# Optimization experiments

Measured on AMD Instinct MI355X. Metric: run time of the kernel, lower is better.

## Reference

```python
import jax, jax.numpy as jnp
import numpy as np

N = 100000          # nodes
E = 1600000         # edges
IN_FEATS = 128
OUT_FEATS = 32      # per head
NUM_HEADS = 8
NEG_SLOPE = 0.2     # DGL GATConv default leaky_relu slope


def setup_inputs() -> dict:
    key = jax.random.key(0)
    k_feat, k_src, k_dst, k_w, k_al, k_ar = jax.random.split(key, 6)
    feat = jax.random.normal(k_feat, (N, IN_FEATS), dtype=jnp.float32)
    src = jax.random.randint(k_src, (E,), 0, N, dtype=jnp.int32)
    dst = jax.random.randint(k_dst, (E,), 0, N, dtype=jnp.int32)
    # learned params of GATConv (fc weight, attn vectors, output bias)
    W = jax.random.normal(k_w, (IN_FEATS, NUM_HEADS * OUT_FEATS), dtype=jnp.float32) * 0.05
    attn_l = jax.random.normal(k_al, (NUM_HEADS, OUT_FEATS), dtype=jnp.float32) * 0.05
    attn_r = jax.random.normal(k_ar, (NUM_HEADS, OUT_FEATS), dtype=jnp.float32) * 0.05
    bias = jnp.zeros((NUM_HEADS * OUT_FEATS,), dtype=jnp.float32)
    return {"feat": feat, "src": src, "dst": dst, "W": W,
            "attn_l": attn_l, "attn_r": attn_r, "bias": bias}


def reference(feat, src, dst, W, attn_l, attn_r, bias):
    # Linear projection: [N, H, D]
    ft = (feat @ W).reshape(N, NUM_HEADS, OUT_FEATS)
    # Per-node attention logit halves: [N, H]
    el = jnp.einsum('nhd,hd->nh', ft, attn_l)
    er = jnp.einsum('nhd,hd->nh', ft, attn_r)
    # Per-edge raw score: [E, H]
    e = jax.nn.leaky_relu(el[src] + er[dst], NEG_SLOPE)
    # Edge softmax over incoming edges of each dst node (segment softmax)
    e_max = jax.ops.segment_max(e, dst, num_segments=N)          # [N, H]
    e_exp = jnp.exp(e - e_max[dst])                              # [E, H]
    e_sum = jax.ops.segment_sum(e_exp, dst, num_segments=N)     # [N, H]
    a = e_exp / e_sum[dst]                                       # [E, H]
    # Weighted message aggregation: [N, H, D]
    msg = ft[src] * a[:, :, None]                                # [E, H, D]
    rst = jax.ops.segment_sum(msg, dst, num_segments=N)
    rst = rst + bias.reshape(NUM_HEADS, OUT_FEATS)
    # Head mean (wrapper): [N, D]
    h = rst.mean(axis=1)
    attn = a[:, :, None]                                         # [E, H, 1] as in DGL
    return (h, attn)
```

## Files before the change

### kernel.cpp

```cpp
#include <hip/hip_runtime.h>
#include <hip/hip_bf16.h>

#define NN 100000
#define NE 1600000
#define KF 128
#define CT 256
#define NH 8
#define SL 56
#define GB 1563

typedef __attribute__((ext_vector_type(8))) short short8;
typedef __attribute__((ext_vector_type(4))) float f32x4;

__device__ __forceinline__ float bf2f(unsigned short u) {
  union { unsigned int i; float f; } x; x.i = ((unsigned int)u) << 16; return x.f;
}
__device__ __forceinline__ unsigned short f2bf(float f) {
  unsigned int b = __float_as_uint(f);
  b += 0x7fffu + ((b >> 16) & 1u);
  return (unsigned short)(b >> 16);
}
__device__ __forceinline__ float lrelu(float e) { return (e > 0.f) ? e : 0.2f * e; }

__global__ void k_wconv(const float* __restrict__ W, unsigned short* __restrict__ Wt) {
  int i = blockIdx.x * 256 + threadIdx.x;
  if (i < KF * CT) {
    int k = i >> 8, c = i & 255;
    Wt[c * KF + k] = f2bf(W[i]);
  }
}

__global__ __launch_bounds__(256) void k_uber(
    const float* __restrict__ feat, const unsigned short* __restrict__ Wt,
    const float* __restrict__ attn_l, const float* __restrict__ attn_r,
    unsigned short* __restrict__ ftb, float* __restrict__ el, float* __restrict__ ei,
    const int* __restrict__ src, const int* __restrict__ dst,
    int* __restrict__ cnt, int* __restrict__ csr)
{
  __shared__ unsigned short fs[64][136];
  const int bid = blockIdx.x;
  const int tid = threadIdx.x;

  if (bid & 1) {
    const int stride = GB * 256;
    for (int e = (bid >> 1) * 256 + tid; e < NE; e += stride) {
      int d = dst[e];
      int sv = src[e];
      int p = atomicAdd(&cnt[d << 4], 1);
      if (p < SL) csr[d * SL + p] = sv;
    }
    return;
  }

  const int lane = tid & 63, w = tid >> 6;
  const int row0 = (bid >> 1) * 64;

  for (int i = tid; i < 64 * 32; i += 256) {
    int r = i >> 5, c4 = (i & 31) * 4;
    int gr = row0 + r;
    float4 v = make_float4(0.f, 0.f, 0.f, 0.f);
    if (gr < NN) v = *(const float4*)(feat + (size_t)gr * KF + c4);
    *(ushort4*)(&fs[r][c4]) = make_ushort4(f2bf(v.x), f2bf(v.y), f2bf(v.z), f2bf(v.w));
  }

  const int bc = lane & 15;
  const int bk = (lane >> 4) * 8;
  short8 bfrag[4][4];
#pragma unroll
  for (int ks = 0; ks < 4; ks++)
#pragma unroll
    for (int n = 0; n < 4; n++)
      bfrag[ks][n] = *(const short8*)(Wt + (size_t)(w * 64 + n * 16 + bc) * KF + ks * 32 + bk);

  __syncthreads();

  f32x4 acc[4][4];
#pragma unroll
  for (int m = 0; m < 4; m++)
#pragma unroll
    for (int n = 0; n < 4; n++) acc[m][n] = (f32x4){0.f, 0.f, 0.f, 0.f};

#pragma unroll
  for (int ks = 0; ks < 4; ks++) {
    short8 af[4];
#pragma unroll
    for (int m = 0; m < 4; m++)
      af[m] = *(const short8*)(&fs[m * 16 + bc][ks * 32 + bk]);
#pragma unroll
    for (int m = 0; m < 4; m++)
#pragma unroll
      for (int n = 0; n < 4; n++)
        acc[m][n] = __builtin_amdgcn_mfma_f32_16x16x32_bf16(af[m], bfrag[ks][n], acc[m][n], 0, 0, 0);
  }

  const int rbase = (lane >> 4) * 4;

#pragma unroll
  for (int m = 0; m < 4; m++) {
#pragma unroll
    for (int r = 0; r < 4; r++) {
      int gr = row0 + m * 16 + rbase + r;
      if (gr < NN) {
        unsigned short* op = ftb + (size_t)gr * CT + w * 64 + bc;
#pragma unroll
        for (int n = 0; n < 4; n++) op[n * 16] = f2bf(acc[m][n][r]);
      }
    }
  }

  float al[4], ar[4];
#pragma unroll
  for (int n = 0; n < 4; n++) {
    al[n] = attn_l[w * 64 + n * 16 + bc];
    ar[n] = attn_r[w * 64 + n * 16 + bc];
  }
#pragma unroll
  for (int m = 0; m < 4; m++) {
#pragma unroll
    for (int r = 0; r < 4; r++) {
      float pl0 = acc[m][0][r] * al[0] + acc[m][1][r] * al[1];
      float pl1 = acc[m][2][r] * al[2] + acc[m][3][r] * al[3];
      float pr0 = acc[m][0][r] * ar[0] + acc[m][1][r] * ar[1];
      float pr1 = acc[m][2][r] * ar[2] + acc[m][3][r] * ar[3];
#pragma unroll
      for (int d = 1; d < 16; d <<= 1) {
        pl0 += __shfl_xor(pl0, d);
        pl1 += __shfl_xor(pl1, d);
        pr0 += __shfl_xor(pr0, d);
        pr1 += __shfl_xor(pr1, d);
      }
      if (bc == 0) {
        int gr = row0 + m * 16 + rbase + r;
        if (gr < NN) {
          *(float2*)(el + (size_t)gr * NH + 2 * w) = make_float2(pl0, pl1);
          *(float2*)(ei + (size_t)gr * 16 + 2 * w) = make_float2(pr0, pr1);
        }
      }
    }
  }
}

__global__ __launch_bounds__(256) void k_edge(
    const int* __restrict__ cnt, const int* __restrict__ csr,
    const float* __restrict__ el, float* __restrict__ ei,
    const unsigned short* __restrict__ ftb, const float* __restrict__ bias,
    float* __restrict__ hout)
{
  const int wid = threadIdx.x >> 6;
  const int lane = threadIdx.x & 63;
  const int n = blockIdx.x * 4 + wid;
  if (n >= NN) return;
  int deg = cnt[n << 4];
  if (deg > SL) deg = SL;
  const int beg = n * SL;

  if (deg == 0) {
    if (lane < 8) {
      ei[(size_t)n * 16 + 8 + lane] = 0.f;
      float b0 = 0.f, b1 = 0.f, b2 = 0.f, b3 = 0.f;
#pragma unroll
      for (int hh = 0; hh < NH; hh++) {
        const float* bp = bias + hh * 32 + lane * 4;
        b0 += bp[0]; b1 += bp[1]; b2 += bp[2]; b3 += bp[3];
      }
      float* op = hout + (size_t)n * 32 + lane * 4;
      *(float4*)op = make_float4(b0 * 0.125f, b1 * 0.125f, b2 * 0.125f, b3 * 0.125f);
    }
    return;
  }

  const int h = lane & 7;
  const int q = lane >> 3;
  const float er_v = ei[(size_t)n * 16 + h];

  const int cv = csr[beg + ((lane < SL) ? lane : 0)];

  const int NG = (deg + 7) >> 3;

  float elv[7];
#pragma unroll
  for (int g = 0; g < 7; g++) {
    elv[g] = 0.f;
    if (g < NG) {
      int si = g * 8 + q; si = (si < deg) ? si : (deg - 1);
      int sn = __shfl(cv, si);
      elv[g] = el[(size_t)sn * NH + h];
    }
  }

  float acc0 = 0.f, acc1 = 0.f, acc2 = 0.f, acc3 = 0.f;
  float wsum = 0.f;
  ushort4 ub0[8], ub1[8];

#pragma unroll
  for (int j = 0; j < 8; j++) {
    int si = (j < deg) ? j : (deg - 1);
    int sj = __shfl(cv, si);
    ub0[j] = *(const ushort4*)(ftb + (size_t)sj * CT + lane * 4);
  }
  if (1 < NG) {
#pragma unroll
    for (int j = 0; j < 8; j++) {
      int si = 8 + j; si = (si < deg) ? si : (deg - 1);
      int sj = __shfl(cv, si);
      ub1[j] = *(const ushort4*)(ftb + (size_t)sj * CT + lane * 4);
    }
  }

#pragma unroll
  for (int g = 0; g < 7; g++) {
    if (g < NG) {
      int s = g * 8 + q;
      float e = lrelu(elv[g] + er_v);
      float wv = (s < deg) ? __expf(e) : 0.f;
      wsum += wv;
      float av[8];
#pragma unroll
      for (int j = 0; j < 8; j++) av[j] = __shfl(wv, j * 8 + q);
      if ((g & 1) == 0) {
#pragma unroll
        for (int j = 0; j < 8; j++) {
          acc0 += bf2f(ub0[j].x) * av[j];
          acc1 += bf2f(ub0[j].y) * av[j];
          acc2 += bf2f(ub0[j].z) * av[j];
          acc3 += bf2f(ub0[j].w) * av[j];
        }
        if (g + 2 < NG) {
#pragma unroll
          for (int j = 0; j < 8; j++) {
            int si = (g + 2) * 8 + j; si = (si < deg) ? si : (deg - 1);
            int sj = __shfl(cv, si);
            ub0[j] = *(const ushort4*)(ftb + (size_t)sj * CT + lane * 4);
          }
        }
      } else {
#pragma unroll
        for (int j = 0; j < 8; j++) {
          acc0 += bf2f(ub1[j].x) * av[j];
          acc1 += bf2f(ub1[j].y) * av[j];
          acc2 += bf2f(ub1[j].z) * av[j];
          acc3 += bf2f(ub1[j].w) * av[j];
        }
        if (g + 2 < NG) {
#pragma unroll
          for (int j = 0; j < 8; j++) {
            int si = (g + 2) * 8 + j; si = (si < deg) ? si : (deg - 1);
            int sj = __shfl(cv, si);
            ub1[j] = *(const ushort4*)(ftb + (size_t)sj * CT + lane * 4);
          }
        }
      }
    }
  }

  wsum += __shfl_xor(wsum, 8); wsum += __shfl_xor(wsum, 16); wsum += __shfl_xor(wsum, 32);
  const float inv = 1.f / wsum;
  if (lane < 8) ei[(size_t)n * 16 + 8 + lane] = inv;

  const float invh = __shfl(inv, q);
  acc0 *= invh; acc1 *= invh; acc2 *= invh; acc3 *= invh;

#pragma unroll
  for (int mks = 8; mks <= 32; mks <<= 1) {
    acc0 += __shfl_xor(acc0, mks);
    acc1 += __shfl_xor(acc1, mks);
    acc2 += __shfl_xor(acc2, mks);
    acc3 += __shfl_xor(acc3, mks);
  }
  if (lane < 8) {
    float b0 = 0.f, b1 = 0.f, b2 = 0.f, b3 = 0.f;
#pragma unroll
    for (int hh = 0; hh < NH; hh++) {
      const float* bp = bias + hh * 32 + lane * 4;
      b0 += bp[0]; b1 += bp[1]; b2 += bp[2]; b3 += bp[3];
    }
    float* op = hout + (size_t)n * 32 + lane * 4;
    __builtin_nontemporal_store((acc0 + b0) * 0.125f, op + 0);
    __builtin_nontemporal_store((acc1 + b1) * 0.125f, op + 1);
    __builtin_nontemporal_store((acc2 + b2) * 0.125f, op + 2);
    __builtin_nontemporal_store((acc3 + b3) * 0.125f, op + 3);
  }
}

__global__ __launch_bounds__(256) void k_attn(
    const int* __restrict__ src, const int* __restrict__ dst,
    const float* __restrict__ el, const float* __restrict__ ei,
    float* __restrict__ attn_out)
{
  int e = blockIdx.x * 256 + threadIdx.x;
  if (e >= NE) return;
  int s = src[e], d = dst[e];
  const float* lp = el + (size_t)s * NH;
  const float* dp = ei + (size_t)d * 16;
  float4 l0 = *(const float4*)(lp);
  float4 l1 = *(const float4*)(lp + 4);
  float4 r0 = *(const float4*)(dp);
  float4 r1 = *(const float4*)(dp + 4);
  float4 i0 = *(const float4*)(dp + 8);
  float4 i1 = *(const float4*)(dp + 12);
  float4 a0, a1;
  a0.x = __expf(lrelu(l0.x + r0.x)) * i0.x;
  a0.y = __expf(lrelu(l0.y + r0.y)) * i0.y;
  a0.z = __expf(lrelu(l0.z + r0.z)) * i0.z;
  a0.w = __expf(lrelu(l0.w + r0.w)) * i0.w;
  a1.x = __expf(lrelu(l1.x + r1.x)) * i1.x;
  a1.y = __expf(lrelu(l1.y + r1.y)) * i1.y;
  a1.z = __expf(lrelu(l1.z + r1.z)) * i1.z;
  a1.w = __expf(lrelu(l1.w + r1.w)) * i1.w;
  float* op = attn_out + (size_t)e * NH;
  __builtin_nontemporal_store(a0.x, op + 0);
  __builtin_nontemporal_store(a0.y, op + 1);
  __builtin_nontemporal_store(a0.z, op + 2);
  __builtin_nontemporal_store(a0.w, op + 3);
  __builtin_nontemporal_store(a1.x, op + 4);
  __builtin_nontemporal_store(a1.y, op + 5);
  __builtin_nontemporal_store(a1.z, op + 6);
  __builtin_nontemporal_store(a1.w, op + 7);
}

extern "C" void kernel_launch(void* const* d_in, const int* in_sizes, int n_in,
                              void* d_out, int out_size, void* d_ws, size_t ws_size,
                              hipStream_t stream) {
  const float* feat   = (const float*)d_in[0];
  const int*   src    = (const int*)d_in[1];
  const int*   dst    = (const int*)d_in[2];
  const float* W      = (const float*)d_in[3];
  const float* attn_l = (const float*)d_in[4];
  const float* attn_r = (const float*)d_in[5];
  const float* bias   = (const float*)d_in[6];

  char* ws = (char*)d_ws;
  size_t o = 0;
  unsigned short* ftb = (unsigned short*)(ws + o); o += (size_t)NN * CT * 2;
  int* csr            = (int*)(ws + o);            o += (size_t)NN * SL * 4;
  float* el           = (float*)(ws + o);          o += (size_t)NN * NH * 4;
  float* ei           = (float*)(ws + o);          o += (size_t)NN * 16 * 4;
  int* cnt            = (int*)(ws + o);            o += (size_t)NN * 64;
  unsigned short* Wt  = (unsigned short*)(ws + o); o += (size_t)CT * KF * 2;

  float* hout     = (float*)d_out;
  float* attn_out = hout + (size_t)NN * 32;

  hipMemsetAsync(cnt, 0, (size_t)NN * 64, stream);
  k_wconv<<<(KF * CT + 255) / 256, 256, 0, stream>>>(W, Wt);
  k_uber<<<GB * 2, 256, 0, stream>>>(feat, Wt, attn_l, attn_r, ftb, el, ei, src, dst, cnt, csr);
  k_edge<<<(NN + 3) / 4, 256, 0, stream>>>(cnt, csr, el, ei, ftb, bias, hout);
  k_attn<<<(NE + 255) / 256, 256, 0, stream>>>(src, dst, el, ei, attn_out);
}
```

Before: 274.3 us.

## Split CSR build and edge aggregation by dst range to overlap stages

Partitions destination nodes at a split point. The first part of the CSR scatter runs alongside the GEMM, and the rest of the scatter runs in the same kernel as aggregation for the first node range. The attention-output pass for those nodes then runs alongside aggregation for the remaining nodes. The cnt array drops its 64-byte padding per counter, which shrinks the memset but brings back atomic contention on shared cache lines. Each scatter and attention pass now reads dst for every edge while only processing its own range, so index reads increase.

Result: slower. 324.2 us (+18.2%).

```diff
diff --git a/kernel.cpp b/kernel.cpp
--- a/kernel.cpp
+++ b/kernel.cpp
@@ -8,6 +8,10 @@
 #define NH 8
 #define SL 56
 #define GB 1563
+#define S_SPLIT 57600
+#define SB2 1024
+#define AB3 1024
+#define EB2 10600
 
 typedef __attribute__((ext_vector_type(8))) short short8;
 typedef __attribute__((ext_vector_type(4))) float f32x4;
@@ -22,135 +26,31 @@
 }
 __device__ __forceinline__ float lrelu(float e) { return (e > 0.f) ? e : 0.2f * e; }
 
-__global__ void k_wconv(const float* __restrict__ W, unsigned short* __restrict__ Wt) {
-  int i = blockIdx.x * 256 + threadIdx.x;
-  if (i < KF * CT) {
-    int k = i >> 8, c = i & 255;
-    Wt[c * KF + k] = f2bf(W[i]);
-  }
-}
-
-__global__ __launch_bounds__(256) void k_uber(
-    const float* __restrict__ feat, const unsigned short* __restrict__ Wt,
-    const float* __restrict__ attn_l, const float* __restrict__ attn_r,
-    unsigned short* __restrict__ ftb, float* __restrict__ el, float* __restrict__ ei,
-    const int* __restrict__ src, const int* __restrict__ dst,
-    int* __restrict__ cnt, int* __restrict__ csr)
-{
-  __shared__ unsigned short fs[64][136];
-  const int bid = blockIdx.x;
-  const int tid = threadIdx.x;
-
-  if (bid & 1) {
-    const int stride = GB * 256;
-    for (int e = (bid >> 1) * 256 + tid; e < NE; e += stride) {
-      int d = dst[e];
+
+__device__ __forceinline__ void scatter_range(
+    const int* __restrict__ src, const int* __restrict__ dst,
+    int* __restrict__ cnt, int* __restrict__ csr,
+    int blk, int nblocks, int lo, int hi, int tid)
+{
+  const int stride = nblocks * 256;
+  for (int e = blk * 256 + tid; e < NE; e += stride) {
+    int d = dst[e];
+    if (d >= lo && d < hi) {
       int sv = src[e];
-      int p = atomicAdd(&cnt[d << 4], 1);
+      int p = atomicAdd(&cnt[d], 1);
       if (p < SL) csr[d * SL + p] = sv;
     }
-    return;
-  }
-
-  const int lane = tid & 63, w = tid >> 6;
-  const int row0 = (bid >> 1) * 64;
-
-  for (int i = tid; i < 64 * 32; i += 256) {
-    int r = i >> 5, c4 = (i & 31) * 4;
-    int gr = row0 + r;
-    float4 v = make_float4(0.f, 0.f, 0.f, 0.f);
-    if (gr < NN) v = *(const float4*)(feat + (size_t)gr * KF + c4);
-    *(ushort4*)(&fs[r][c4]) = make_ushort4(f2bf(v.x), f2bf(v.y), f2bf(v.z), f2bf(v.w));
-  }
-
-  const int bc = lane & 15;
-  const int bk = (lane >> 4) * 8;
-  short8 bfrag[4][4];
-#pragma unroll
-  for (int ks = 0; ks < 4; ks++)
-#pragma unroll
-    for (int n = 0; n < 4; n++)
-      bfrag[ks][n] = *(const short8*)(Wt + (size_t)(w * 64 + n * 16 + bc) * KF + ks * 32 + bk);
-
-  __syncthreads();
-
-  f32x4 acc[4][4];
-#pragma unroll
-  for (int m = 0; m < 4; m++)
-#pragma unroll
-    for (int n = 0; n < 4; n++) acc[m][n] = (f32x4){0.f, 0.f, 0.f, 0.f};
-
-#pragma unroll
-  for (int ks = 0; ks < 4; ks++) {
-    short8 af[4];
-#pragma unroll
-    for (int m = 0; m < 4; m++)
-      af[m] = *(const short8*)(&fs[m * 16 + bc][ks * 32 + bk]);
-#pragma unroll
-    for (int m = 0; m < 4; m++)
-#pragma unroll
-      for (int n = 0; n < 4; n++)
-        acc[m][n] = __builtin_amdgcn_mfma_f32_16x16x32_bf16(af[m], bfrag[ks][n], acc[m][n], 0, 0, 0);
-  }
-
-  const int rbase = (lane >> 4) * 4;
-
-#pragma unroll
-  for (int m = 0; m < 4; m++) {
-#pragma unroll
-    for (int r = 0; r < 4; r++) {
-      int gr = row0 + m * 16 + rbase + r;
-      if (gr < NN) {
-        unsigned short* op = ftb + (size_t)gr * CT + w * 64 + bc;
-#pragma unroll
-        for (int n = 0; n < 4; n++) op[n * 16] = f2bf(acc[m][n][r]);
-      }
-    }
-  }
-
-  float al[4], ar[4];
-#pragma unroll
-  for (int n = 0; n < 4; n++) {
-    al[n] = attn_l[w * 64 + n * 16 + bc];
-    ar[n] = attn_r[w * 64 + n * 16 + bc];
-  }
-#pragma unroll
-  for (int m = 0; m < 4; m++) {
-#pragma unroll
-    for (int r = 0; r < 4; r++) {
-      float pl0 = acc[m][0][r] * al[0] + acc[m][1][r] * al[1];
-      float pl1 = acc[m][2][r] * al[2] + acc[m][3][r] * al[3];
-      float pr0 = acc[m][0][r] * ar[0] + acc[m][1][r] * ar[1];
-      float pr1 = acc[m][2][r] * ar[2] + acc[m][3][r] * ar[3];
-#pragma unroll
-      for (int d = 1; d < 16; d <<= 1) {
-        pl0 += __shfl_xor(pl0, d);
-        pl1 += __shfl_xor(pl1, d);
-        pr0 += __shfl_xor(pr0, d);
-        pr1 += __shfl_xor(pr1, d);
-      }
-      if (bc == 0) {
-        int gr = row0 + m * 16 + rbase + r;
-        if (gr < NN) {
-          *(float2*)(el + (size_t)gr * NH + 2 * w) = make_float2(pl0, pl1);
-          *(float2*)(ei + (size_t)gr * 16 + 2 * w) = make_float2(pr0, pr1);
-        }
-      }
-    }
-  }
-}
-
-__global__ __launch_bounds__(256) void k_edge(
+  }
+}
+
+__device__ __forceinline__ void edge_node(
+    int n, int lane,
     const int* __restrict__ cnt, const int* __restrict__ csr,
     const float* __restrict__ el, float* __restrict__ ei,
     const unsigned short* __restrict__ ftb, const float* __restrict__ bias,
     float* __restrict__ hout)
 {
-  const int wid = threadIdx.x >> 6;
-  const int lane = threadIdx.x & 63;
-  const int n = blockIdx.x * 4 + wid;
-  if (n >= NN) return;
-  int deg = cnt[n << 4];
+  int deg = cnt[n];
   if (deg > SL) deg = SL;
   const int beg = n * SL;
 
@@ -172,9 +72,7 @@
   const int h = lane & 7;
   const int q = lane >> 3;
   const float er_v = ei[(size_t)n * 16 + h];
-
   const int cv = csr[beg + ((lane < SL) ? lane : 0)];
-
   const int NG = (deg + 7) >> 3;
 
   float elv[7];
@@ -282,14 +180,11 @@
   }
 }
 
-__global__ __launch_bounds__(256) void k_attn(
-    const int* __restrict__ src, const int* __restrict__ dst,
+__device__ __forceinline__ void attn_edge(
+    int e, int s, int d,
     const float* __restrict__ el, const float* __restrict__ ei,
     float* __restrict__ attn_out)
 {
-  int e = blockIdx.x * 256 + threadIdx.x;
-  if (e >= NE) return;
-  int s = src[e], d = dst[e];
   const float* lp = el + (size_t)s * NH;
   const float* dp = ei + (size_t)d * 16;
   float4 l0 = *(const float4*)(lp);
@@ -298,24 +193,178 @@
   float4 r1 = *(const float4*)(dp + 4);
   float4 i0 = *(const float4*)(dp + 8);
   float4 i1 = *(const float4*)(dp + 12);
-  float4 a0, a1;
-  a0.x = __expf(lrelu(l0.x + r0.x)) * i0.x;
-  a0.y = __expf(lrelu(l0.y + r0.y)) * i0.y;
-  a0.z = __expf(lrelu(l0.z + r0.z)) * i0.z;
-  a0.w = __expf(lrelu(l0.w + r0.w)) * i0.w;
-  a1.x = __expf(lrelu(l1.x + r1.x)) * i1.x;
-  a1.y = __expf(lrelu(l1.y + r1.y)) * i1.y;
-  a1.z = __expf(lrelu(l1.z + r1.z)) * i1.z;
-  a1.w = __expf(lrelu(l1.w + r1.w)) * i1.w;
   float* op = attn_out + (size_t)e * NH;
-  __builtin_nontemporal_store(a0.x, op + 0);
-  __builtin_nontemporal_store(a0.y, op + 1);
-  __builtin_nontemporal_store(a0.z, op + 2);
-  __builtin_nontemporal_store(a0.w, op + 3);
-  __builtin_nontemporal_store(a1.x, op + 4);
-  __builtin_nontemporal_store(a1.y, op + 5);
-  __builtin_nontemporal_store(a1.z, op + 6);
-  __builtin_nontemporal_store(a1.w, op + 7);
+  __builtin_nontemporal_store(__expf(lrelu(l0.x + r0.x)) * i0.x, op + 0);
+  __builtin_nontemporal_store(__expf(lrelu(l0.y + r0.y)) * i0.y, op + 1);
+  __builtin_nontemporal_store(__expf(lrelu(l0.z + r0.z)) * i0.z, op + 2);
+  __builtin_nontemporal_store(__expf(lrelu(l0.w + r0.w)) * i0.w, op + 3);
+  __builtin_nontemporal_store(__expf(lrelu(l1.x + r1.x)) * i1.x, op + 4);
+  __builtin_nontemporal_store(__expf(lrelu(l1.y + r1.y)) * i1.y, op + 5);
+  __builtin_nontemporal_store(__expf(lrelu(l1.z + r1.z)) * i1.z, op + 6);
+  __builtin_nontemporal_store(__expf(lrelu(l1.w + r1.w)) * i1.w, op + 7);
+}
+
+__global__ void k_wconv(const float* __restrict__ W, unsigned short* __restrict__ Wt) {
+  int i = blockIdx.x * 256 + threadIdx.x;
+  if (i < KF * CT) {
+    int k = i >> 8, c = i & 255;
+    Wt[c * KF + k] = f2bf(W[i]);
+  }
+}
+
+__global__ __launch_bounds__(256) void k_uber(
+    const float* __restrict__ feat, const unsigned short* __restrict__ Wt,
+    const float* __restrict__ attn_l, const float* __restrict__ attn_r,
+    unsigned short* __restrict__ ftb, float* __restrict__ el, float* __restrict__ ei,
+    const int* __restrict__ src, const int* __restrict__ dst,
+    int* __restrict__ cnt, int* __restrict__ csr)
+{
+  __shared__ unsigned short fs[64][136];
+  const int bid = blockIdx.x;
+  const int tid = threadIdx.x;
+
+  if (bid & 1) {
+    scatter_range(src, dst, cnt, csr, bid >> 1, GB, 0, S_SPLIT, tid);
+    return;
+  }
+
+  const int lane = tid & 63, w = tid >> 6;
+  const int row0 = (bid >> 1) * 64;
+
+  for (int i = tid; i < 64 * 32; i += 256) {
+    int r = i >> 5, c4 = (i & 31) * 4;
+    int gr = row0 + r;
+    float4 v = make_float4(0.f, 0.f, 0.f, 0.f);
+    if (gr < NN) v = *(const float4*)(feat + (size_t)gr * KF + c4);
+    *(ushort4*)(&fs[r][c4]) = make_ushort4(f2bf(v.x), f2bf(v.y), f2bf(v.z), f2bf(v.w));
+  }
+
+  const int bc = lane & 15;
+  const int bk = (lane >> 4) * 8;
+  short8 bfrag[4][4];
+#pragma unroll
+  for (int ks = 0; ks < 4; ks++)
+#pragma unroll
+    for (int n = 0; n < 4; n++)
+      bfrag[ks][n] = *(const short8*)(Wt + (size_t)(w * 64 + n * 16 + bc) * KF + ks * 32 + bk);
+
+  __syncthreads();
+
+  f32x4 acc[4][4];
+#pragma unroll
+  for (int m = 0; m < 4; m++)
+#pragma unroll
+    for (int n = 0; n < 4; n++) acc[m][n] = (f32x4){0.f, 0.f, 0.f, 0.f};
+
+#pragma unroll
+  for (int ks = 0; ks < 4; ks++) {
+    short8 af[4];
+#pragma unroll
+    for (int m = 0; m < 4; m++)
+      af[m] = *(const short8*)(&fs[m * 16 + bc][ks * 32 + bk]);
+#pragma unroll
+    for (int m = 0; m < 4; m++)
+#pragma unroll
+      for (int n = 0; n < 4; n++)
+        acc[m][n] = __builtin_amdgcn_mfma_f32_16x16x32_bf16(af[m], bfrag[ks][n], acc[m][n], 0, 0, 0);
+  }
+
+  const int rbase = (lane >> 4) * 4;
+
+#pragma unroll
+  for (int m = 0; m < 4; m++) {
+#pragma unroll
+    for (int r = 0; r < 4; r++) {
+      int gr = row0 + m * 16 + rbase + r;
+      if (gr < NN) {
+        unsigned short* op = ftb + (size_t)gr * CT + w * 64 + bc;
+#pragma unroll
+        for (int n = 0; n < 4; n++) op[n * 16] = f2bf(acc[m][n][r]);
+      }
+    }
+  }
+
+  float al[4], ar[4];
+#pragma unroll
+  for (int n = 0; n < 4; n++) {
+    al[n] = attn_l[w * 64 + n * 16 + bc];
+    ar[n] = attn_r[w * 64 + n * 16 + bc];
+  }
+#pragma unroll
+  for (int m = 0; m < 4; m++) {
+#pragma unroll
+    for (int r = 0; r < 4; r++) {
+      float pl0 = acc[m][0][r] * al[0] + acc[m][1][r] * al[1];
+      float pl1 = acc[m][2][r] * al[2] + acc[m][3][r] * al[3];
+      float pr0 = acc[m][0][r] * ar[0] + acc[m][1][r] * ar[1];
+      float pr1 = acc[m][2][r] * ar[2] + acc[m][3][r] * ar[3];
+#pragma unroll
+      for (int d = 1; d < 16; d <<= 1) {
+        pl0 += __shfl_xor(pl0, d);
+        pl1 += __shfl_xor(pl1, d);
+        pr0 += __shfl_xor(pr0, d);
+        pr1 += __shfl_xor(pr1, d);
+      }
+      if (bc == 0) {
+        int gr = row0 + m * 16 + rbase + r;
+        if (gr < NN) {
+          *(float2*)(el + (size_t)gr * NH + 2 * w) = make_float2(pl0, pl1);
+          *(float2*)(ei + (size_t)gr * 16 + 2 * w) = make_float2(pr0, pr1);
+        }
+      }
+    }
+  }
+}
+
+__global__ __launch_bounds__(256) void k_mid(
+    const int* __restrict__ src, const int* __restrict__ dst,
+    int* __restrict__ cnt, int* __restrict__ csr,
+    const float* __restrict__ el, float* __restrict__ ei,
+    const unsigned short* __restrict__ ftb, const float* __restrict__ bias,
+    float* __restrict__ hout)
+{
+  const int bid = blockIdx.x;
+  if (bid < SB2) {
+    scatter_range(src, dst, cnt, csr, bid, SB2, S_SPLIT, NN, threadIdx.x);
+    return;
+  }
+  const int n = (bid - SB2) * 4 + (threadIdx.x >> 6);
+  if (n < S_SPLIT)
+    edge_node(n, threadIdx.x & 63, cnt, csr, el, ei, ftb, bias, hout);
+}
+
+__global__ __launch_bounds__(256) void k_fin(
+    const int* __restrict__ src, const int* __restrict__ dst,
+    const int* __restrict__ cnt, const int* __restrict__ csr,
+    const float* __restrict__ el, float* __restrict__ ei,
+    const unsigned short* __restrict__ ftb, const float* __restrict__ bias,
+    float* __restrict__ hout, float* __restrict__ attn_out)
+{
+  const int bid = blockIdx.x;
+  if (bid < EB2) {
+    const int n = S_SPLIT + bid * 4 + (threadIdx.x >> 6);
+    if (n < NN)
+      edge_node(n, threadIdx.x & 63, cnt, csr, el, ei, ftb, bias, hout);
+    return;
+  }
+  const int blk = bid - EB2;
+  const int stride = AB3 * 256;
+  for (int e = blk * 256 + threadIdx.x; e < NE; e += stride) {
+    int d = dst[e];
+    if (d < S_SPLIT) attn_edge(e, src[e], d, el, ei, attn_out);
+  }
+}
+
+__global__ __launch_bounds__(256) void k_attn2(
+    const int* __restrict__ src, const int* __restrict__ dst,
+    const float* __restrict__ el, const float* __restrict__ ei,
+    float* __restrict__ attn_out)
+{
+  int e = blockIdx.x * 256 + threadIdx.x;
+  if (e < NE) {
+    int d = dst[e];
+    if (d >= S_SPLIT) attn_edge(e, src[e], d, el, ei, attn_out);
+  }
 }
 
 extern "C" void kernel_launch(void* const* d_in, const int* in_sizes, int n_in,
@@ -335,15 +384,16 @@
   int* csr            = (int*)(ws + o);            o += (size_t)NN * SL * 4;
   float* el           = (float*)(ws + o);          o += (size_t)NN * NH * 4;
   float* ei           = (float*)(ws + o);          o += (size_t)NN * 16 * 4;
-  int* cnt            = (int*)(ws + o);            o += (size_t)NN * 64;
+  int* cnt            = (int*)(ws + o);            o += (size_t)NN * 4;
   unsigned short* Wt  = (unsigned short*)(ws + o); o += (size_t)CT * KF * 2;
 
   float* hout     = (float*)d_out;
   float* attn_out = hout + (size_t)NN * 32;
 
-  hipMemsetAsync(cnt, 0, (size_t)NN * 64, stream);
+  hipMemsetAsync(cnt, 0, (size_t)NN * sizeof(int), stream);
   k_wconv<<<(KF * CT + 255) / 256, 256, 0, stream>>>(W, Wt);
   k_uber<<<GB * 2, 256, 0, stream>>>(feat, Wt, attn_l, attn_r, ftb, el, ei, src, dst, cnt, csr);
-  k_edge<<<(NN + 3) / 4, 256, 0, stream>>>(cnt, csr, el, ei, ftb, bias, hout);
-  k_attn<<<(NE + 255) / 256, 256, 0, stream>>>(src, dst, el, ei, attn_out);
-}
+  k_mid<<<SB2 + S_SPLIT / 4, 256, 0, stream>>>(src, dst, cnt, csr, el, ei, ftb, bias, hout);
+  k_fin<<<EB2 + AB3, 256, 0, stream>>>(src, dst, cnt, csr, el, ei, ftb, bias, hout, attn_out);
+  k_attn2<<<(NE + 255) / 256, 256, 0, stream>>>(src, dst, el, ei, attn_out);
+}
```

## Partition CSR-build atomics by XCD-local dst slices and pack counters densely

Applied to the files above, without the earlier changes.

The CSR-building blocks of the fused kernel are split into 8 classes by block index. Each class scans all edges but only inserts those whose destination falls in its slice, selected by (d>>4)&7. This appears intended to keep each destination's atomic counter traffic on one XCD's L2. The per-node counters go from 64-byte padding to dense ints, which shrinks the memset and the counter footprint. The cost is that every scatter block now reads all of dst, which is 8x the dst read traffic.

Measured after the change: 395.5 us. 1.44x slower.

```diff
diff --git a/kernel.cpp b/kernel.cpp
--- a/kernel.cpp
+++ b/kernel.cpp
@@ -8,6 +8,8 @@
 #define NH 8
 #define SL 56
 #define GB 1563
+#define GSLOT 1568
+#define SCB 196
 
 typedef __attribute__((ext_vector_type(8))) short short8;
 typedef __attribute__((ext_vector_type(4))) float f32x4;
@@ -41,19 +43,25 @@
   const int bid = blockIdx.x;
   const int tid = threadIdx.x;
 
-  if (bid & 1) {
-    const int stride = GB * 256;
-    for (int e = (bid >> 1) * 256 + tid; e < NE; e += stride) {
+  if ((bid >> 3) & 1) {
+    const int c = bid & 7;
+    const int s = bid >> 4;
+    const int stride = SCB * 256;
+    for (int e = s * 256 + tid; e < NE; e += stride) {
       int d = dst[e];
-      int sv = src[e];
-      int p = atomicAdd(&cnt[d << 4], 1);
-      if (p < SL) csr[d * SL + p] = sv;
+      if (((d >> 4) & 7) == c) {
+        int sv = src[e];
+        int p = atomicAdd(&cnt[d], 1);
+        if (p < SL) csr[d * SL + p] = sv;
+      }
     }
     return;
   }
 
+  const int t = (bid >> 4) * 8 + (bid & 7);
+  if (t >= GB) return;
   const int lane = tid & 63, w = tid >> 6;
-  const int row0 = (bid >> 1) * 64;
+  const int row0 = t * 64;
 
   for (int i = tid; i < 64 * 32; i += 256) {
     int r = i >> 5, c4 = (i & 31) * 4;
@@ -150,7 +158,7 @@
   const int lane = threadIdx.x & 63;
   const int n = blockIdx.x * 4 + wid;
   if (n >= NN) return;
-  int deg = cnt[n << 4];
+  int deg = cnt[n];
   if (deg > SL) deg = SL;
   const int beg = n * SL;
 
@@ -172,9 +180,7 @@
   const int h = lane & 7;
   const int q = lane >> 3;
   const float er_v = ei[(size_t)n * 16 + h];
-
   const int cv = csr[beg + ((lane < SL) ? lane : 0)];
-
   const int NG = (deg + 7) >> 3;
 
   float elv[7];
@@ -298,24 +304,15 @@
   float4 r1 = *(const float4*)(dp + 4);
   float4 i0 = *(const float4*)(dp + 8);
   float4 i1 = *(const float4*)(dp + 12);
-  float4 a0, a1;
-  a0.x = __expf(lrelu(l0.x + r0.x)) * i0.x;
-  a0.y = __expf(lrelu(l0.y + r0.y)) * i0.y;
-  a0.z = __expf(lrelu(l0.z + r0.z)) * i0.z;
-  a0.w = __expf(lrelu(l0.w + r0.w)) * i0.w;
-  a1.x = __expf(lrelu(l1.x + r1.x)) * i1.x;
-  a1.y = __expf(lrelu(l1.y + r1.y)) * i1.y;
-  a1.z = __expf(lrelu(l1.z + r1.z)) * i1.z;
-  a1.w = __expf(lrelu(l1.w + r1.w)) * i1.w;
   float* op = attn_out + (size_t)e * NH;
-  __builtin_nontemporal_store(a0.x, op + 0);
-  __builtin_nontemporal_store(a0.y, op + 1);
-  __builtin_nontemporal_store(a0.z, op + 2);
-  __builtin_nontemporal_store(a0.w, op + 3);
-  __builtin_nontemporal_store(a1.x, op + 4);
-  __builtin_nontemporal_store(a1.y, op + 5);
-  __builtin_nontemporal_store(a1.z, op + 6);
-  __builtin_nontemporal_store(a1.w, op + 7);
+  __builtin_nontemporal_store(__expf(lrelu(l0.x + r0.x)) * i0.x, op + 0);
+  __builtin_nontemporal_store(__expf(lrelu(l0.y + r0.y)) * i0.y, op + 1);
+  __builtin_nontemporal_store(__expf(lrelu(l0.z + r0.z)) * i0.z, op + 2);
+  __builtin_nontemporal_store(__expf(lrelu(l0.w + r0.w)) * i0.w, op + 3);
+  __builtin_nontemporal_store(__expf(lrelu(l1.x + r1.x)) * i1.x, op + 4);
+  __builtin_nontemporal_store(__expf(lrelu(l1.y + r1.y)) * i1.y, op + 5);
+  __builtin_nontemporal_store(__expf(lrelu(l1.z + r1.z)) * i1.z, op + 6);
+  __builtin_nontemporal_store(__expf(lrelu(l1.w + r1.w)) * i1.w, op + 7);
 }
 
 extern "C" void kernel_launch(void* const* d_in, const int* in_sizes, int n_in,
@@ -335,15 +332,15 @@
   int* csr            = (int*)(ws + o);            o += (size_t)NN * SL * 4;
   float* el           = (float*)(ws + o);          o += (size_t)NN * NH * 4;
   float* ei           = (float*)(ws + o);          o += (size_t)NN * 16 * 4;
-  int* cnt            = (int*)(ws + o);            o += (size_t)NN * 64;
+  int* cnt            = (int*)(ws + o);            o += (size_t)NN * 4;
   unsigned short* Wt  = (unsigned short*)(ws + o); o += (size_t)CT * KF * 2;
 
   float* hout     = (float*)d_out;
   float* attn_out = hout + (size_t)NN * 32;
 
-  hipMemsetAsync(cnt, 0, (size_t)NN * 64, stream);
+  hipMemsetAsync(cnt, 0, (size_t)NN * sizeof(int), stream);
   k_wconv<<<(KF * CT + 255) / 256, 256, 0, stream>>>(W, Wt);
-  k_uber<<<GB * 2, 256, 0, stream>>>(feat, Wt, attn_l, attn_r, ftb, el, ei, src, dst, cnt, csr);
+  k_uber<<<GSLOT * 2, 256, 0, stream>>>(feat, Wt, attn_l, attn_r, ftb, el, ei, src, dst, cnt, csr);
   k_edge<<<(NN + 3) / 4, 256, 0, stream>>>(cnt, csr, el, ei, ftb, bias, hout);
   k_attn<<<(NE + 255) / 256, 256, 0, stream>>>(src, dst, el, ei, attn_out);
 }
```
